# Performance work log

Hardware: AMD Instinct MI355X
Metric: run time of the kernel (lower is better)

## Reference

```python
import jax, jax.numpy as jnp
import numpy as np

LN_EPS = 1e-12


def _layernorm(x, g, b):
    mu = jnp.mean(x, axis=-1, keepdims=True)
    var = jnp.mean(jnp.square(x - mu), axis=-1, keepdims=True)
    return (x - mu) * jax.lax.rsqrt(var + LN_EPS) * g + b


def setup_inputs() -> dict:
    key = jax.random.key(0)
    ks = jax.random.split(key, 8)
    A, EP, H, HI, D = 64, 8, 768, 1536, 100
    Etot = A * EP
    return {
        "E": jax.random.normal(ks[0], (A, Etot, H), dtype=jnp.float32),
        "W1": jax.random.normal(ks[1], (H, HI), dtype=jnp.float32) * 0.02,
        "b1": jnp.zeros((HI,), jnp.float32),
        "ln_g": jnp.ones((HI,), jnp.float32),
        "ln_b": jnp.zeros((HI,), jnp.float32),
        "W2": jax.random.normal(ks[2], (HI, D), dtype=jnp.float32) * 0.02,
        "b2": jnp.zeros((D,), jnp.float32),
        "entity_count": 8,  # uniform entities per step (static)
    }


def reference(E, W1, b1, ln_g, ln_b, W2, b2, entity_count):
    A, Etot, H = E.shape
    EP = int(entity_count)
    D = W2.shape[1]

    # VG head: Linear -> exact GELU -> LayerNorm(eps=1e-12) -> Linear
    h = E.reshape(-1, H) @ W1 + b1                       # [A*Etot, 2H]
    h = _layernorm(jax.nn.gelu(h, approximate=False), ln_g, ln_b)
    logits = h @ W2 + b2                                 # [A*Etot, D]
    # reshape(A, Etot, D).permute(1,0,2) -> [Etot, A, D]
    VG_logits = logits.reshape(A, Etot, D).transpose(1, 0, 2)

    # per-entity logits at its own step: idx_2 = step index of each entity
    steps_of = jnp.arange(Etot) // EP                    # [Etot]
    own = VG_logits[jnp.arange(Etot), steps_of]          # [Etot, D]
    VG_scores = jnp.max(jax.nn.softmax(own, axis=-1), axis=-1)  # [Etot]
    VG_scores_index = jnp.argmax(own, axis=-1)           # [Etot] (argmax of softmax == argmax of logits)

    # Faithful to original loop: b stays -1 (`bbox = b+1` never updates b),
    # so every valid score gathers detection VG_scores_index[-1].
    sel = VG_scores_index[-1]
    # entity e=(m,j) -> VG_logits[e, l, sel]; uniform counts => all (j,k) valid
    g = VG_logits[:, :, sel].reshape(A, EP, A)           # [m, j, l]
    scores = jnp.broadcast_to(
        g.transpose(2, 0, 1)[:, :, :, None], (A, A, EP, EP)
    )                                                    # [l, m, j, k]
    scores = scores[None]                                # [1, A, A, EP, EP]

    VG_scores_index_padded = VG_scores_index.reshape(A, EP)
    return scores, VG_scores, VG_scores_index_padded
```

## Files before the change

### kernel.cpp

```cpp
#include <hip/hip_runtime.h>
#include <hip/hip_bf16.h>
#include <math.h>


typedef __bf16 bf16_t;
typedef __bf16  bf16x2  __attribute__((ext_vector_type(2)));
typedef __bf16  bf16x8  __attribute__((ext_vector_type(8)));
typedef float   floatx4 __attribute__((ext_vector_type(4)));

__device__ __forceinline__ float gelu_exact(float x) {
    return 0.5f * x * (1.0f + erff(x * 0.7071067811865475f));
}
__device__ __forceinline__ float gelu_fast(float x) {
    const float z = x * (1.0f + 0.044715f * x * x);
    return __fdividef(x, 1.0f + __expf(-1.5957691216f * z));
}

__device__ __forceinline__ void gl_lds16(const void* g, void* l) {
    __builtin_amdgcn_global_load_lds(
        (const __attribute__((address_space(1))) void*)g,
        (__attribute__((address_space(3))) void*)l, 16, 0, 0);
}

__global__ __launch_bounds__(256) void prep_duo(
        const float* __restrict__ E, const float* __restrict__ W1,
        bf16_t* __restrict__ W1t, float* __restrict__ hpart,
        bf16_t* __restrict__ Ebf) {
    __shared__ alignas(16) char smemc[16640];
    const int bid = blockIdx.x;
    const int tid = threadIdx.x;

    if (bid >= 1056) {
        const int cb = bid - 1056;
        const size_t base = ((size_t)cb * 256 + tid) * 8;
        const float4 v0 = *(const float4*)(E + base);
        const float4 v1 = *(const float4*)(E + base + 4);
        bf16x8 o;
        o[0] = (bf16_t)v0.x; o[1] = (bf16_t)v0.y;
        o[2] = (bf16_t)v0.z; o[3] = (bf16_t)v0.w;
        o[4] = (bf16_t)v1.x; o[5] = (bf16_t)v1.y;
        o[6] = (bf16_t)v1.z; o[7] = (bf16_t)v1.w;
        *(bf16x8*)(Ebf + base) = o;
        return;
    }

    if (bid < 288) {
        float* sT = (float*)smemc;
        const int bk = bid % 12, bn = bid / 12;
        const int k0 = bk * 64, n0 = bn * 64;
        #pragma unroll
        for (int i = 0; i < 16; ++i) {
            const int idx = tid + i * 256;
            const int kk = idx >> 6, nn = idx & 63;
            sT[kk * 65 + nn] = W1[(size_t)(k0 + kk) * 1536 + n0 + nn];
        }
        __syncthreads();
        #pragma unroll
        for (int i = 0; i < 8; ++i) {
            const int idx = tid + i * 256;
            const int nn = idx >> 5;
            const int kp = (idx & 31) * 2;
            bf16x2 v;
            v[0] = (bf16_t)sT[kp * 65 + nn];
            v[1] = (bf16_t)sT[(kp + 1) * 65 + nn];
            *(bf16x2*)(W1t + (size_t)(n0 + nn) * 768 + k0 + kp) = v;
        }
    } else {
        float* sE = (float*)smemc;
        const int b  = bid - 288;
        const int a  = b & 63;
        const int rest = b >> 6;
        const int by = rest % 3, kq = rest / 3;

        const float* Ebase = E + (size_t)(520 * a) * 768 + kq * 192;
        for (int idx = tid; idx < 1536; idx += 256) {
            const int row = idx / 192, i = idx - row * 192;
            sE[idx] = Ebase[(size_t)row * 768 + i];
        }
        __syncthreads();

        const int c0 = by * 512 + tid * 2;
        const float* w1p = W1 + (size_t)(kq * 192) * 1536 + c0;
        float ax[8] = {}, ay[8] = {};
        for (int k = 0; k < 192; ++k) {
            const float2 w = *(const float2*)(w1p + (size_t)k * 1536);
            #pragma unroll
            for (int j = 0; j < 8; ++j) {
                const float e = sE[j * 192 + k];
                ax[j] += w.x * e;
                ay[j] += w.y * e;
            }
        }
        #pragma unroll
        for (int j = 0; j < 8; ++j)
            *(float2*)(hpart + (size_t)(kq * 512 + a * 8 + j) * 1536 + c0)
                = make_float2(ax[j], ay[j]);
    }
}

__global__ __launch_bounds__(512) void own_lnlog(
        const float* __restrict__ hpart, const float* __restrict__ b1,
        const float* __restrict__ lng,  const float* __restrict__ lnb,
        const float* __restrict__ W2,   const float* __restrict__ b2,
        float* __restrict__ out, float* __restrict__ u,
        float* __restrict__ gwbw) {
    __shared__ float srow[1536];
    __shared__ float red16[16];
    __shared__ float redl[384];
    __shared__ float slog[128];
    __shared__ int   ssel;
    const int row = blockIdx.x, tid = threadIdx.x;
    const int lane = tid & 63, wv = tid >> 6;

    float x[3];
    #pragma unroll
    for (int i = 0; i < 3; ++i) {
        const int c = tid + i * 512;
        x[i] = gelu_exact(hpart[(size_t)row * 1536 + c]
                        + hpart[(size_t)(512 + row) * 1536 + c]
                        + hpart[(size_t)(1024 + row) * 1536 + c]
                        + hpart[(size_t)(1536 + row) * 1536 + c] + b1[c]);
    }
    float s = x[0] + x[1] + x[2];
    #pragma unroll
    for (int o = 32; o > 0; o >>= 1) s += __shfl_xor(s, o, 64);
    if (lane == 0) red16[wv] = s;
    __syncthreads();
    float mu = 0.f;
    #pragma unroll
    for (int i = 0; i < 8; ++i) mu += red16[i];
    mu *= (1.0f / 1536.0f);

    float s2 = 0.f;
    #pragma unroll
    for (int i = 0; i < 3; ++i) { float d = x[i] - mu; s2 += d * d; }
    #pragma unroll
    for (int o = 32; o > 0; o >>= 1) s2 += __shfl_xor(s2, o, 64);
    if (lane == 0) red16[8 + wv] = s2;
    __syncthreads();
    float v2 = 0.f;
    #pragma unroll
    for (int i = 0; i < 8; ++i) v2 += red16[8 + i];
    const float rstd = rsqrtf(v2 * (1.0f / 1536.0f) + 1e-12f);

    #pragma unroll
    for (int i = 0; i < 3; ++i) {
        const int c = tid + i * 512;
        srow[c] = (x[i] - mu) * rstd * lng[c] + lnb[c];
    }
    __syncthreads();

    const int d  = tid & 127;
    const int ks = tid >> 7;
    const int dd = d < 100 ? d : 99;
    float acc = (ks == 0) ? b2[dd] : 0.0f;
    const float* hr  = srow + ks * 384;
    const float* w2p = W2 + (size_t)(ks * 384) * 100 + dd;
    #pragma unroll 8
    for (int k = 0; k < 384; ++k)
        acc += hr[k] * w2p[(size_t)k * 100];
    if (ks) redl[(ks - 1) * 128 + d] = acc;
    __syncthreads();
    if (ks == 0) {
        const float tot = acc + redl[d] + redl[128 + d] + redl[256 + d];
        slog[d] = (d < 100) ? tot : -INFINITY;
    }
    __syncthreads();

    if (wv == 0) {
        const float v0 = slog[lane], v1 = slog[lane + 64];
        float bv; int bi;
        if (v0 >= v1) { bv = v0; bi = lane; } else { bv = v1; bi = lane + 64; }
        #pragma unroll
        for (int o = 1; o < 64; o <<= 1) {
            const float vo = __shfl_xor(bv, o, 64);
            const int   io = __shfl_xor(bi, o, 64);
            if (vo > bv || (vo == bv && io < bi)) { bv = vo; bi = io; }
        }
        float e = expf(v0 - bv) + expf(v1 - bv);
        #pragma unroll
        for (int o = 32; o > 0; o >>= 1) e += __shfl_xor(e, o, 64);
        if (lane == 0) {
            out[262144 + row] = 1.0f / e;
            out[262656 + row] = (float)bi;
            ssel = bi;
        }
    }
    __syncthreads();

    if (row == 511) {
        const int sel = ssel;
        float gw = 0.f, bw = 0.f;
        #pragma unroll
        for (int c = tid; c < 1536; c += 512) {
            const float wv2 = W2[(size_t)c * 100 + sel];
            const float uu = lng[c] * wv2;
            u[c] = uu;
            gw += uu;
            bw += lnb[c] * wv2;
        }
        #pragma unroll
        for (int o = 32; o > 0; o >>= 1) {
            gw += __shfl_xor(gw, o, 64);
            bw += __shfl_xor(bw, o, 64);
        }
        if (lane == 0) { red16[wv] = gw; red16[8 + wv] = bw; }
        __syncthreads();
        if (tid == 0) {
            float G = 0.f, B = 0.f;
            #pragma unroll
            for (int i = 0; i < 8; ++i) { G += red16[i]; B += red16[8 + i]; }
            gwbw[0] = G;
            gwbw[1] = B + b2[sel];
        }
    }
}

__global__ __launch_bounds__(256) void gemm1p(
        const bf16_t* __restrict__ A, const bf16_t* __restrict__ Bt,
        const float* __restrict__ bias, const float* __restrict__ u,
        float* __restrict__ pS1, float* __restrict__ pS2,
        float* __restrict__ pD) {
    constexpr int K = 768;
    __shared__ alignas(16) char smem[36864];
    bf16_t* sA = (bf16_t*)smem;
    bf16_t* sB = (bf16_t*)(smem + 16384);

    const int linear = blockIdx.x + gridDim.x * blockIdx.y;
    const int xcd  = linear & 7;
    const int slot = linear >> 3;
    const int bx = slot % gridDim.x;
    const int by = (slot / gridDim.x) * 8 + xcd;

    const int tid  = threadIdx.x;
    const int lane = tid & 63;
    const int wave = tid >> 6;
    const int wr = wave >> 1, wc = wave & 1;
    const int m0 = by * 128;
    const int n0 = bx * 128;
    const int q  = lane >> 4;
    const int l15 = lane & 15;

    const bf16_t* gA[4]; bf16_t* lA[4];
    const bf16_t* gB[4]; bf16_t* lB[4];
    #pragma unroll
    for (int c = 0; c < 4; ++c) {
        const int s    = c * 256 + tid;
        const int row  = s >> 3;
        const int col  = s & 7;
        const int gcol = col ^ (row & 7);
        gA[c] = A  + (size_t)(m0 + row) * K + gcol * 8;
        lA[c] = sA + (c * 256 + wave * 64) * 8;
        gB[c] = Bt + (size_t)(n0 + row) * K + gcol * 8;
        lB[c] = sB + (c * 256 + wave * 64) * 8;
    }
    const bf16_t* rA[4]; const bf16_t* rB[4];
    #pragma unroll
    for (int t4 = 0; t4 < 4; ++t4) {
        rA[t4] = sA + (wr * 64 + t4 * 16 + l15) * 64;
        rB[t4] = sB + (wc * 64 + t4 * 16 + l15) * 64;
    }
    const int c0 = ((q)     ^ (lane & 7)) * 8;
    const int c1 = ((4 + q) ^ (lane & 7)) * 8;

    floatx4 acc[4][4] = {};

    #pragma unroll
    for (int kt = 0; kt < 12; ++kt) {
        const int k0 = kt * 64;
        __syncthreads();
        #pragma unroll
        for (int c = 0; c < 4; ++c) gl_lds16(gB[c] + k0, lB[c]);
        #pragma unroll
        for (int c = 0; c < 4; ++c) gl_lds16(gA[c] + k0, lA[c]);
        __syncthreads();

        #pragma unroll
        for (int ks = 0; ks < 2; ++ks) {
            const int co = ks ? c1 : c0;
            bf16x8 af[4], bfr[4];
            #pragma unroll
            for (int t4 = 0; t4 < 4; ++t4) {
                af[t4]  = *(const bf16x8*)(rA[t4] + co);
                bfr[t4] = *(const bf16x8*)(rB[t4] + co);
            }
            #pragma unroll
            for (int mt = 0; mt < 4; ++mt)
                #pragma unroll
                for (int nt = 0; nt < 4; ++nt)
                    acc[mt][nt] = __builtin_amdgcn_mfma_f32_16x16x32_bf16(
                        af[mt], bfr[nt], acc[mt][nt], 0, 0, 0);
        }
    }

    __syncthreads();
    bf16_t* sh = (bf16_t*)smem;
    float*  su = (float*)(smem + 33280);
    float*  sp = (float*)(smem + 33792);

    if (tid < 128) su[tid] = u[n0 + tid];
    float bias4[4];
    #pragma unroll
    for (int nt = 0; nt < 4; ++nt) bias4[nt] = bias[n0 + wc * 64 + nt * 16 + l15];

    #pragma unroll
    for (int mt = 0; mt < 4; ++mt)
        #pragma unroll
        for (int nt = 0; nt < 4; ++nt)
            #pragma unroll
            for (int r = 0; r < 4; ++r) {
                const int rowl = wr * 64 + mt * 16 + q * 4 + r;
                const int coll = wc * 64 + nt * 16 + l15;
                sh[rowl * 130 + coll] = (bf16_t)gelu_fast(acc[mt][nt][r] + bias4[nt]);
            }
    __syncthreads();

    {
        const int rowl = tid >> 1, half = tid & 1;
        const bf16_t* hp = sh + rowl * 130 + half * 64;
        const float*  up = su + half * 64;
        float s1 = 0.f, s2 = 0.f, dd = 0.f;
        #pragma unroll
        for (int c = 0; c < 64; ++c) {
            const float v = (float)hp[c];
            s1 += v; s2 += v * v; dd += v * up[c];
        }
        sp[tid * 3 + 0] = s1; sp[tid * 3 + 1] = s2; sp[tid * 3 + 2] = dd;
    }
    __syncthreads();
    if (tid < 128) {
        const float* p0 = sp + (2 * tid) * 3;
        const float* p1 = sp + (2 * tid + 1) * 3;
        const size_t idx = (size_t)bx * 32768 + (m0 + tid);
        pS1[idx] = p0[0] + p1[0];
        pS2[idx] = p0[1] + p1[1];
        pD[idx]  = p0[2] + p1[2];
    }
}

__global__ __launch_bounds__(256) void out_scores(
        const float* __restrict__ pS1, const float* __restrict__ pS2,
        const float* __restrict__ pD,  const float* __restrict__ gwbw,
        float* __restrict__ out) {
    const int t = blockIdx.x * 256 + threadIdx.x;
    float s1 = 0.f, s2 = 0.f, d = 0.f;
    #pragma unroll
    for (int nt = 0; nt < 12; ++nt) {
        const size_t idx = (size_t)nt * 32768 + t;
        s1 += pS1[idx]; s2 += pS2[idx]; d += pD[idx];
    }
    const float mu   = s1 * (1.0f / 1536.0f);
    const float var  = s2 * (1.0f / 1536.0f) - mu * mu;
    const float rstd = rsqrtf(var + 1e-12f);
    const float v = rstd * (d - mu * gwbw[0]) + gwbw[1];
    const float4 f = make_float4(v, v, v, v);
    float4* o = (float4*)(out + (size_t)t * 8);
    o[0] = f; o[1] = f;
}

extern "C" void kernel_launch(void* const* d_in, const int* in_sizes, int n_in,
                              void* d_out, int out_size, void* d_ws, size_t ws_size,
                              hipStream_t stream) {
    const float* E   = (const float*)d_in[0];
    const float* W1  = (const float*)d_in[1];
    const float* b1  = (const float*)d_in[2];
    const float* lng = (const float*)d_in[3];
    const float* lnb = (const float*)d_in[4];
    const float* W2  = (const float*)d_in[5];
    const float* b2  = (const float*)d_in[6];
    float* out = (float*)d_out;

    char* w = (char*)d_ws;
    auto carve = [&](size_t bytes) {
        void* p = (void*)w;
        w += (bytes + 255) & ~(size_t)255;
        return p;
    };
    bf16_t* W1t   = (bf16_t*)carve((size_t)1536 * 768 * 2);
    bf16_t* Ebf   = (bf16_t*)carve((size_t)32768 * 768 * 2);
    float*  u     = (float*)carve(1536 * 4);
    float*  gwbw  = (float*)carve(256);
    char*   unionr = (char*)carve((size_t)4 * 512 * 1536 * 4);
    float*  hpart = (float*)unionr;
    float*  pS1   = (float*)unionr;
    float*  pS2   = (float*)(unionr + (size_t)12 * 32768 * 4);
    float*  pD    = (float*)(unionr + (size_t)24 * 32768 * 4);

    prep_duo<<<13344, 256, 0, stream>>>(E, W1, W1t, hpart, Ebf);
    own_lnlog<<<512, 512, 0, stream>>>(hpart, b1, lng, lnb, W2, b2,
                                       out, u, gwbw);
    gemm1p<<<dim3(12, 256), 256, 0, stream>>>(Ebf, W1t, b1, u, pS1, pS2, pD);
    out_scores<<<128, 256, 0, stream>>>(pS1, pS2, pD, gwbw, out);
}
```

Before: 305.7 us.

## Merge own-row LayerNorm logits into GEMM launch and split out row-511 finalizer

Replaces the 512-block own_lnlog kernel with a single-block kernel that only computes the selected index and the u/gwbw vectors from row 511. The per-row GELU/LayerNorm/logit/softmax work for the 512 own rows is now done by 512 extra blocks prepended to the GEMM grid, so that work can overlap with the GEMM tiles. The GEMM grid becomes 1D with explicit XCD remapping. hpart and the GEMM partial buffers no longer alias, because they are now live at the same time. This costs extra workspace, and a serial single-block launch now sits on the critical path.

```diff
diff --git a/kernel.cpp b/kernel.cpp
--- a/kernel.cpp
+++ b/kernel.cpp
@@ -98,18 +98,17 @@
     }
 }
 
-__global__ __launch_bounds__(512) void own_lnlog(
+__global__ __launch_bounds__(512) void row511_fin(
         const float* __restrict__ hpart, const float* __restrict__ b1,
         const float* __restrict__ lng,  const float* __restrict__ lnb,
         const float* __restrict__ W2,   const float* __restrict__ b2,
-        float* __restrict__ out, float* __restrict__ u,
-        float* __restrict__ gwbw) {
+        float* __restrict__ u, float* __restrict__ gwbw) {
     __shared__ float srow[1536];
     __shared__ float red16[16];
     __shared__ float redl[384];
     __shared__ float slog[128];
     __shared__ int   ssel;
-    const int row = blockIdx.x, tid = threadIdx.x;
+    const int row = 511, tid = threadIdx.x;
     const int lane = tid & 63, wv = tid >> 6;
 
     float x[3];
@@ -177,62 +176,134 @@
             const int   io = __shfl_xor(bi, o, 64);
             if (vo > bv || (vo == bv && io < bi)) { bv = vo; bi = io; }
         }
-        float e = expf(v0 - bv) + expf(v1 - bv);
-        #pragma unroll
-        for (int o = 32; o > 0; o >>= 1) e += __shfl_xor(e, o, 64);
-        if (lane == 0) {
-            out[262144 + row] = 1.0f / e;
-            out[262656 + row] = (float)bi;
-            ssel = bi;
-        }
-    }
-    __syncthreads();
-
-    if (row == 511) {
-        const int sel = ssel;
-        float gw = 0.f, bw = 0.f;
-        #pragma unroll
-        for (int c = tid; c < 1536; c += 512) {
-            const float wv2 = W2[(size_t)c * 100 + sel];
-            const float uu = lng[c] * wv2;
-            u[c] = uu;
-            gw += uu;
-            bw += lnb[c] * wv2;
-        }
-        #pragma unroll
-        for (int o = 32; o > 0; o >>= 1) {
-            gw += __shfl_xor(gw, o, 64);
-            bw += __shfl_xor(bw, o, 64);
-        }
-        if (lane == 0) { red16[wv] = gw; red16[8 + wv] = bw; }
-        __syncthreads();
-        if (tid == 0) {
-            float G = 0.f, B = 0.f;
-            #pragma unroll
-            for (int i = 0; i < 8; ++i) { G += red16[i]; B += red16[8 + i]; }
-            gwbw[0] = G;
-            gwbw[1] = B + b2[sel];
-        }
-    }
-}
-
-__global__ __launch_bounds__(256) void gemm1p(
+        if (lane == 0) ssel = bi;
+    }
+    __syncthreads();
+
+    const int sel = ssel;
+    float gw = 0.f, bw = 0.f;
+    #pragma unroll
+    for (int c = tid; c < 1536; c += 512) {
+        const float wv2 = W2[(size_t)c * 100 + sel];
+        const float uu = lng[c] * wv2;
+        u[c] = uu;
+        gw += uu;
+        bw += lnb[c] * wv2;
+    }
+    #pragma unroll
+    for (int o = 32; o > 0; o >>= 1) {
+        gw += __shfl_xor(gw, o, 64);
+        bw += __shfl_xor(bw, o, 64);
+    }
+    if (lane == 0) { red16[wv] = gw; red16[8 + wv] = bw; }
+    __syncthreads();
+    if (tid == 0) {
+        float G = 0.f, B = 0.f;
+        #pragma unroll
+        for (int i = 0; i < 8; ++i) { G += red16[i]; B += red16[8 + i]; }
+        gwbw[0] = G;
+        gwbw[1] = B + b2[sel];
+    }
+}
+
+__global__ __launch_bounds__(256) void gemm_own(
         const bf16_t* __restrict__ A, const bf16_t* __restrict__ Bt,
         const float* __restrict__ bias, const float* __restrict__ u,
         float* __restrict__ pS1, float* __restrict__ pS2,
-        float* __restrict__ pD) {
+        float* __restrict__ pD,
+        const float* __restrict__ hpart, const float* __restrict__ lng,
+        const float* __restrict__ lnb,  const float* __restrict__ W2,
+        const float* __restrict__ b2,   float* __restrict__ out) {
     constexpr int K = 768;
     __shared__ alignas(16) char smem[36864];
+    const int bid = blockIdx.x;
+    const int tid = threadIdx.x;
+
+    if (bid < 512) {
+        const int row = bid;
+        float* srow = (float*)smem;
+        float* red8 = (float*)(smem + 6144);
+        float* redl = (float*)(smem + 6208);
+        float* slog = (float*)(smem + 6720);
+        const int lane = tid & 63, wv = tid >> 6;
+
+        float x[6];
+        #pragma unroll
+        for (int i = 0; i < 6; ++i) {
+            const int c = tid + i * 256;
+            x[i] = gelu_exact(hpart[(size_t)row * 1536 + c]
+                            + hpart[(size_t)(512 + row) * 1536 + c]
+                            + hpart[(size_t)(1024 + row) * 1536 + c]
+                            + hpart[(size_t)(1536 + row) * 1536 + c] + bias[c]);
+        }
+        float s = 0.f;
+        #pragma unroll
+        for (int i = 0; i < 6; ++i) s += x[i];
+        #pragma unroll
+        for (int o = 32; o > 0; o >>= 1) s += __shfl_xor(s, o, 64);
+        if (lane == 0) red8[wv] = s;
+        __syncthreads();
+        const float mu = (red8[0] + red8[1] + red8[2] + red8[3]) * (1.0f / 1536.0f);
+
+        float s2 = 0.f;
+        #pragma unroll
+        for (int i = 0; i < 6; ++i) { float dx = x[i] - mu; s2 += dx * dx; }
+        #pragma unroll
+        for (int o = 32; o > 0; o >>= 1) s2 += __shfl_xor(s2, o, 64);
+        if (lane == 0) red8[4 + wv] = s2;
+        __syncthreads();
+        const float rstd = rsqrtf((red8[4] + red8[5] + red8[6] + red8[7])
+                                  * (1.0f / 1536.0f) + 1e-12f);
+
+        #pragma unroll
+        for (int i = 0; i < 6; ++i) {
+            const int c = tid + i * 256;
+            srow[c] = (x[i] - mu) * rstd * lng[c] + lnb[c];
+        }
+        __syncthreads();
+
+        const int d  = tid & 127;
+        const int ks = tid >> 7;
+        const int dd = d < 100 ? d : 99;
+        float acc = ks ? 0.0f : b2[dd];
+        const float* hr = srow + ks * 768;
+        for (int k = 0; k < 768; ++k)
+            acc += hr[k] * W2[(size_t)(ks * 768 + k) * 100 + dd];
+        if (ks) redl[d] = acc;
+        __syncthreads();
+        if (!ks) slog[d] = (d < 100) ? (acc + redl[d]) : -INFINITY;
+        __syncthreads();
+
+        if (wv == 0) {
+            const float v0 = slog[lane], v1 = slog[lane + 64];
+            float bv; int bi;
+            if (v0 >= v1) { bv = v0; bi = lane; } else { bv = v1; bi = lane + 64; }
+            #pragma unroll
+            for (int o = 1; o < 64; o <<= 1) {
+                const float vo = __shfl_xor(bv, o, 64);
+                const int   io = __shfl_xor(bi, o, 64);
+                if (vo > bv || (vo == bv && io < bi)) { bv = vo; bi = io; }
+            }
+            float e = expf(v0 - bv) + expf(v1 - bv);
+            #pragma unroll
+            for (int o = 32; o > 0; o >>= 1) e += __shfl_xor(e, o, 64);
+            if (lane == 0) {
+                out[262144 + row] = 1.0f / e;
+                out[262656 + row] = (float)bi;
+            }
+        }
+        return;
+    }
+
     bf16_t* sA = (bf16_t*)smem;
     bf16_t* sB = (bf16_t*)(smem + 16384);
 
-    const int linear = blockIdx.x + gridDim.x * blockIdx.y;
-    const int xcd  = linear & 7;
-    const int slot = linear >> 3;
-    const int bx = slot % gridDim.x;
-    const int by = (slot / gridDim.x) * 8 + xcd;
-
-    const int tid  = threadIdx.x;
+    const int g = bid - 512;
+    const int xcd  = g & 7;
+    const int slot = g >> 3;
+    const int bx = slot % 12;
+    const int by = (slot / 12) * 8 + xcd;
+
     const int lane = tid & 63;
     const int wave = tid >> 6;
     const int wr = wave >> 1, wc = wave & 1;
@@ -380,15 +451,14 @@
     bf16_t* Ebf   = (bf16_t*)carve((size_t)32768 * 768 * 2);
     float*  u     = (float*)carve(1536 * 4);
     float*  gwbw  = (float*)carve(256);
-    char*   unionr = (char*)carve((size_t)4 * 512 * 1536 * 4);
-    float*  hpart = (float*)unionr;
-    float*  pS1   = (float*)unionr;
-    float*  pS2   = (float*)(unionr + (size_t)12 * 32768 * 4);
-    float*  pD    = (float*)(unionr + (size_t)24 * 32768 * 4);
+    float*  hpart = (float*)carve((size_t)4 * 512 * 1536 * 4);
+    float*  pS1   = (float*)carve((size_t)12 * 32768 * 4);
+    float*  pS2   = (float*)carve((size_t)12 * 32768 * 4);
+    float*  pD    = (float*)carve((size_t)12 * 32768 * 4);
 
     prep_duo<<<13344, 256, 0, stream>>>(E, W1, W1t, hpart, Ebf);
-    own_lnlog<<<512, 512, 0, stream>>>(hpart, b1, lng, lnb, W2, b2,
-                                       out, u, gwbw);
-    gemm1p<<<dim3(12, 256), 256, 0, stream>>>(Ebf, W1t, b1, u, pS1, pS2, pD);
+    row511_fin<<<1, 512, 0, stream>>>(hpart, b1, lng, lnb, W2, b2, u, gwbw);
+    gemm_own<<<3584, 256, 0, stream>>>(Ebf, W1t, b1, u, pS1, pS2, pD,
+                                       hpart, lng, lnb, W2, b2, out);
     out_scores<<<128, 256, 0, stream>>>(pS1, pS2, pD, gwbw, out);
 }
```

After: 317.0 us. +3.7%, slower.
